# Kernel optimization log

Measured on AMD Instinct MI355X. Metric: run time of the kernel, lower is better.

The kernel has to match this reference:

```python
import jax, jax.numpy as jnp
from jax import lax
import numpy as np

HIDDEN = 64
B, T = 256, 3000


def setup_inputs() -> dict:
    key = jax.random.key(0)
    ks = jax.random.split(key, 7)
    s = 1.0 / np.sqrt(HIDDEN)  # torch default uniform(-1/sqrt(H), 1/sqrt(H))
    u = lambda k, shape: jax.random.uniform(k, shape, jnp.float32, -s, s)
    return {
        "x": jax.random.normal(ks[0], (B, T, 1), dtype=jnp.float32),
        "W_ih": u(ks[1], (3 * HIDDEN, 1)),
        "W_hh": u(ks[2], (3 * HIDDEN, HIDDEN)),
        "b_ih": u(ks[3], (3 * HIDDEN,)),
        "b_hh": u(ks[4], (3 * HIDDEN,)),
        "W_fc": u(ks[5], (1, HIDDEN)),
        "b_fc": u(ks[6], (1,)),
    }


def reference(x, W_ih, W_hh, b_ih, b_hh, W_fc, b_fc):
    # Precompute input contributions to all three gates for all timesteps: (B, T, 3H)
    gi = jnp.einsum("bti,gi->btg", x, W_ih) + b_ih

    def step(h, gi_t):
        gh = h @ W_hh.T + b_hh                      # (B, 3H)
        i_r, i_z, i_n = jnp.split(gi_t, 3, axis=-1)  # torch gate order: r, z, n
        h_r, h_z, h_n = jnp.split(gh, 3, axis=-1)
        r = jax.nn.sigmoid(i_r + h_r)
        z = jax.nn.sigmoid(i_z + h_z)
        n = jnp.tanh(i_n + r * h_n)
        h_new = (1.0 - z) * n + z * h
        return h_new, None

    h0 = jnp.zeros((x.shape[0], HIDDEN), dtype=x.dtype)
    hT, _ = lax.scan(step, h0, jnp.swapaxes(gi, 0, 1))  # scan over T
    # fc(o[:, -1]).squeeze() -> (B,)
    return (hT @ W_fc.T + b_fc).squeeze(-1)
```

## Files before the change

### kernel.cpp

```cpp
#include <hip/hip_runtime.h>
#include <math.h>

#define T_LEN 3000
#define HID 64

typedef _Float16 f16;
typedef f16 f16x8 __attribute__((ext_vector_type(8)));
typedef float f32x4 __attribute__((ext_vector_type(4)));

#define NLOG2E  (-1.4426950408889634f)
#define N2LOG2E (-2.8853900817779268f)

__device__ __forceinline__ float bcast_lane(float v, int j) {
    return __builtin_bit_cast(float,
        __builtin_amdgcn_readlane(__builtin_bit_cast(int, v), j));
}

__global__ __launch_bounds__(256, 1)
void gru_tail(
    const float* __restrict__ x,
    const float* __restrict__ W_ih,
    const float* __restrict__ W_hh,
    const float* __restrict__ b_ih,
    const float* __restrict__ b_hh,
    const float* __restrict__ W_fc,
    const float* __restrict__ b_fc,
    float* __restrict__ out)
{
    const int tid = threadIdx.x;
    const int w   = tid >> 6;
    const int l   = tid & 63;
    const int col = l & 15;
    const int grp = l >> 4;
    const int u   = 16 * w + col;
    const int b   = blockIdx.x;
    const long xbase = (long)b * T_LEN;

    __shared__ __align__(16) f16 hbuf[2][HID];
    __shared__ float hf32[HID];

    f16x8 Bf[3][2];
#pragma unroll
    for (int g = 0; g < 3; ++g) {
#pragma unroll
        for (int hf = 0; hf < 2; ++hf) {
            const float* p = W_hh + (size_t)(64 * g + 16 * w + col) * HID
                           + 8 * grp + 32 * hf;
            const float4 a = *reinterpret_cast<const float4*>(p);
            const float4 c = *reinterpret_cast<const float4*>(p + 4);
            f16x8 v;
            v[0] = (f16)a.x; v[1] = (f16)a.y; v[2] = (f16)a.z; v[3] = (f16)a.w;
            v[4] = (f16)c.x; v[5] = (f16)c.y; v[6] = (f16)c.z; v[7] = (f16)c.w;
            Bf[g][hf] = v;
        }
    }

    const float wihr2 = W_ih[u]        * NLOG2E;
    const float wihz2 = W_ih[64 + u]   * NLOG2E;
    const float wihn2 = W_ih[128 + u]  * N2LOG2E;
    const float br2   = (b_ih[u]        + b_hh[u])        * NLOG2E;
    const float bz2   = (b_ih[64 + u]   + b_hh[64 + u])   * NLOG2E;
    const float bin2  = b_ih[128 + u]  * N2LOG2E;
    const float bhn2  = b_hh[128 + u]  * N2LOG2E;

    float xwin = x[xbase + l];
    float xnxt = (64 + l < T_LEN) ? x[xbase + 64 + l] : 0.0f;

    if (tid < HID) hbuf[0][tid] = (f16)0.0f;
    __syncthreads();

    float h = 0.0f;
    const f32x4 zf = {0.f, 0.f, 0.f, 0.f};

    const f16x8* s0A = reinterpret_cast<const f16x8*>(hbuf[0]) + grp;
    const f16x8* s0B = s0A + 4;
    const f16x8* s1A = reinterpret_cast<const f16x8*>(hbuf[1]) + grp;
    const f16x8* s1B = s1A + 4;
    f16* d0 = &hbuf[0][u];
    f16* d1 = &hbuf[1][u];

    auto step = [&](const f16x8* aP, const f16x8* bP, f16* dstu, int t) {
        const int j = t & 63;

        const f16x8 A0 = *aP;
        const f16x8 A1 = *bP;

        const float xt    = bcast_lane(xwin, j);
        const float pre_r = fmaf(xt, wihr2, br2);
        const float pre_z = fmaf(xt, wihz2, bz2);
        const float pre_n = fmaf(xt, wihn2, bin2);

        f32x4 pr = __builtin_amdgcn_mfma_f32_16x16x32_f16(A0, Bf[0][0], zf, 0, 0, 0);
        f32x4 pz = __builtin_amdgcn_mfma_f32_16x16x32_f16(A0, Bf[1][0], zf, 0, 0, 0);
        f32x4 pn = __builtin_amdgcn_mfma_f32_16x16x32_f16(A0, Bf[2][0], zf, 0, 0, 0);
        f32x4 qr = __builtin_amdgcn_mfma_f32_16x16x32_f16(A1, Bf[0][1], pr, 0, 0, 0);
        f32x4 qz = __builtin_amdgcn_mfma_f32_16x16x32_f16(A1, Bf[1][1], pz, 0, 0, 0);
        f32x4 qn = __builtin_amdgcn_mfma_f32_16x16x32_f16(A1, Bf[2][1], pn, 0, 0, 0);

        const float r = __builtin_amdgcn_rcpf(
            1.0f + __builtin_amdgcn_exp2f(fmaf(qr[0], NLOG2E, pre_r)));
        const float hn2 = fmaf(qn[0], N2LOG2E, bhn2);
        const float z = __builtin_amdgcn_rcpf(
            1.0f + __builtin_amdgcn_exp2f(fmaf(qz[0], NLOG2E, pre_z)));
        const float zh  = z * h;
        const float omz = 1.0f - z;
        const float n = fmaf(2.0f, __builtin_amdgcn_rcpf(
            1.0f + __builtin_amdgcn_exp2f(fmaf(r, hn2, pre_n))), -1.0f);
        h = fmaf(omz, n, zh);

        *dstu = (f16)h;
        if (j == 63) {
            xwin = xnxt;
            const int idx = t + 65 + l;
            xnxt = (idx < T_LEN) ? x[xbase + idx] : 0.0f;
        }
        asm volatile("s_waitcnt lgkmcnt(0)\n\ts_barrier" ::: "memory");
    };

    for (int t = 0; t < T_LEN; t += 2) {
        step(s0A, s0B, d1, t);
        step(s1A, s1B, d0, t + 1);
    }

    hf32[u] = h;
    __syncthreads();
    if (tid < HID) {
        float v = hf32[tid] * W_fc[tid];
#pragma unroll
        for (int off = 32; off > 0; off >>= 1) v += __shfl_down(v, off);
        if (tid == 0) out[b] = v + b_fc[0];
    }
}

extern "C" void kernel_launch(void* const* d_in, const int* in_sizes, int n_in,
                              void* d_out, int out_size, void* d_ws, size_t ws_size,
                              hipStream_t stream) {
    const float* x    = (const float*)d_in[0];
    const float* W_ih = (const float*)d_in[1];
    const float* W_hh = (const float*)d_in[2];
    const float* b_ih = (const float*)d_in[3];
    const float* b_hh = (const float*)d_in[4];
    const float* W_fc = (const float*)d_in[5];
    const float* b_fc = (const float*)d_in[6];
    float* out = (float*)d_out;

    const int B = 256;
    gru_tail<<<B, 256, 0, stream>>>(x, W_ih, W_hh, b_ih, b_hh, W_fc, b_fc, out);
}
```

Before: 636.8 us.

## Replace per-step MFMA matvec with packed fdot2 dot products and quad DPP reduction

```diff
diff --git a/kernel.cpp b/kernel.cpp
--- a/kernel.cpp
+++ b/kernel.cpp
@@ -5,8 +5,8 @@
 #define HID 64
 
 typedef _Float16 f16;
+typedef f16 f16x2 __attribute__((ext_vector_type(2)));
 typedef f16 f16x8 __attribute__((ext_vector_type(8)));
-typedef float f32x4 __attribute__((ext_vector_type(4)));
 
 #define NLOG2E  (-1.4426950408889634f)
 #define N2LOG2E (-2.8853900817779268f)
@@ -16,8 +16,15 @@
         __builtin_amdgcn_readlane(__builtin_bit_cast(int, v), j));
 }
 
+template <int CTRL>
+__device__ __forceinline__ float quad_xor_add(float v) {
+    const int t = __builtin_amdgcn_mov_dpp(
+        __builtin_bit_cast(int, v), CTRL, 0xf, 0xf, true);
+    return v + __builtin_bit_cast(float, t);
+}
+
 __global__ __launch_bounds__(256, 1)
-void gru_tail(
+void gru_qdot(
     const float* __restrict__ x,
     const float* __restrict__ W_ih,
     const float* __restrict__ W_hh,
@@ -30,29 +37,30 @@
     const int tid = threadIdx.x;
     const int w   = tid >> 6;
     const int l   = tid & 63;
-    const int col = l & 15;
-    const int grp = l >> 4;
-    const int u   = 16 * w + col;
+    const int u   = 16 * w + (l >> 2);
+    const int k0  = 16 * (l & 3);
     const int b   = blockIdx.x;
     const long xbase = (long)b * T_LEN;
 
     __shared__ __align__(16) f16 hbuf[2][HID];
     __shared__ float hf32[HID];
 
-    f16x8 Bf[3][2];
+    f16x2 Wd[3][8];
 #pragma unroll
     for (int g = 0; g < 3; ++g) {
-#pragma unroll
-        for (int hf = 0; hf < 2; ++hf) {
-            const float* p = W_hh + (size_t)(64 * g + 16 * w + col) * HID
-                           + 8 * grp + 32 * hf;
-            const float4 a = *reinterpret_cast<const float4*>(p);
-            const float4 c = *reinterpret_cast<const float4*>(p + 4);
-            f16x8 v;
-            v[0] = (f16)a.x; v[1] = (f16)a.y; v[2] = (f16)a.z; v[3] = (f16)a.w;
-            v[4] = (f16)c.x; v[5] = (f16)c.y; v[6] = (f16)c.z; v[7] = (f16)c.w;
-            Bf[g][hf] = v;
-        }
+        const float* p = W_hh + (size_t)(64 * g + u) * HID + k0;
+        const float4 a = *reinterpret_cast<const float4*>(p);
+        const float4 c = *reinterpret_cast<const float4*>(p + 4);
+        const float4 d = *reinterpret_cast<const float4*>(p + 8);
+        const float4 e = *reinterpret_cast<const float4*>(p + 12);
+        Wd[g][0].x = (f16)a.x; Wd[g][0].y = (f16)a.y;
+        Wd[g][1].x = (f16)a.z; Wd[g][1].y = (f16)a.w;
+        Wd[g][2].x = (f16)c.x; Wd[g][2].y = (f16)c.y;
+        Wd[g][3].x = (f16)c.z; Wd[g][3].y = (f16)c.w;
+        Wd[g][4].x = (f16)d.x; Wd[g][4].y = (f16)d.y;
+        Wd[g][5].x = (f16)d.z; Wd[g][5].y = (f16)d.w;
+        Wd[g][6].x = (f16)e.x; Wd[g][6].y = (f16)e.y;
+        Wd[g][7].x = (f16)e.z; Wd[g][7].y = (f16)e.w;
     }
 
     const float wihr2 = W_ih[u]        * NLOG2E;
@@ -70,38 +78,51 @@
     __syncthreads();
 
     float h = 0.0f;
-    const f32x4 zf = {0.f, 0.f, 0.f, 0.f};
 
-    const f16x8* s0A = reinterpret_cast<const f16x8*>(hbuf[0]) + grp;
-    const f16x8* s0B = s0A + 4;
-    const f16x8* s1A = reinterpret_cast<const f16x8*>(hbuf[1]) + grp;
-    const f16x8* s1B = s1A + 4;
+    union HU { f16x8 v8; f16x2 v2[4]; };
+    const f16x8* s0 = reinterpret_cast<const f16x8*>(hbuf[0]) + 2 * (l & 3);
+    const f16x8* s1 = reinterpret_cast<const f16x8*>(hbuf[1]) + 2 * (l & 3);
     f16* d0 = &hbuf[0][u];
     f16* d1 = &hbuf[1][u];
 
-    auto step = [&](const f16x8* aP, const f16x8* bP, f16* dstu, int t) {
+    auto step = [&](const f16x8* srcP, f16* dstu, int t) {
         const int j = t & 63;
 
-        const f16x8 A0 = *aP;
-        const f16x8 A1 = *bP;
+        HU hlo, hhi;
+        hlo.v8 = srcP[0];
+        hhi.v8 = srcP[1];
 
         const float xt    = bcast_lane(xwin, j);
         const float pre_r = fmaf(xt, wihr2, br2);
         const float pre_z = fmaf(xt, wihz2, bz2);
         const float pre_n = fmaf(xt, wihn2, bin2);
 
-        f32x4 pr = __builtin_amdgcn_mfma_f32_16x16x32_f16(A0, Bf[0][0], zf, 0, 0, 0);
-        f32x4 pz = __builtin_amdgcn_mfma_f32_16x16x32_f16(A0, Bf[1][0], zf, 0, 0, 0);
-        f32x4 pn = __builtin_amdgcn_mfma_f32_16x16x32_f16(A0, Bf[2][0], zf, 0, 0, 0);
-        f32x4 qr = __builtin_amdgcn_mfma_f32_16x16x32_f16(A1, Bf[0][1], pr, 0, 0, 0);
-        f32x4 qz = __builtin_amdgcn_mfma_f32_16x16x32_f16(A1, Bf[1][1], pz, 0, 0, 0);
-        f32x4 qn = __builtin_amdgcn_mfma_f32_16x16x32_f16(A1, Bf[2][1], pn, 0, 0, 0);
+        float sr = 0.f, sz = 0.f, sn = 0.f;
+#pragma unroll
+        for (int p = 0; p < 4; ++p) {
+            sr = __builtin_amdgcn_fdot2(Wd[0][p], hlo.v2[p], sr, false);
+            sz = __builtin_amdgcn_fdot2(Wd[1][p], hlo.v2[p], sz, false);
+            sn = __builtin_amdgcn_fdot2(Wd[2][p], hlo.v2[p], sn, false);
+        }
+#pragma unroll
+        for (int p = 0; p < 4; ++p) {
+            sr = __builtin_amdgcn_fdot2(Wd[0][4 + p], hhi.v2[p], sr, false);
+            sz = __builtin_amdgcn_fdot2(Wd[1][4 + p], hhi.v2[p], sz, false);
+            sn = __builtin_amdgcn_fdot2(Wd[2][4 + p], hhi.v2[p], sn, false);
+        }
+
+        sr = quad_xor_add<0xB1>(sr);
+        sz = quad_xor_add<0xB1>(sz);
+        sn = quad_xor_add<0xB1>(sn);
+        sr = quad_xor_add<0x4E>(sr);
+        sz = quad_xor_add<0x4E>(sz);
+        sn = quad_xor_add<0x4E>(sn);
 
         const float r = __builtin_amdgcn_rcpf(
-            1.0f + __builtin_amdgcn_exp2f(fmaf(qr[0], NLOG2E, pre_r)));
-        const float hn2 = fmaf(qn[0], N2LOG2E, bhn2);
+            1.0f + __builtin_amdgcn_exp2f(fmaf(sr, NLOG2E, pre_r)));
+        const float hn2 = fmaf(sn, N2LOG2E, bhn2);
         const float z = __builtin_amdgcn_rcpf(
-            1.0f + __builtin_amdgcn_exp2f(fmaf(qz[0], NLOG2E, pre_z)));
+            1.0f + __builtin_amdgcn_exp2f(fmaf(sz, NLOG2E, pre_z)));
         const float zh  = z * h;
         const float omz = 1.0f - z;
         const float n = fmaf(2.0f, __builtin_amdgcn_rcpf(
@@ -118,8 +139,8 @@
     };
 
     for (int t = 0; t < T_LEN; t += 2) {
-        step(s0A, s0B, d1, t);
-        step(s1A, s1B, d0, t + 1);
+        step(s0, d1, t);
+        step(s1, d0, t + 1);
     }
 
     hf32[u] = h;
@@ -145,5 +166,5 @@
     float* out = (float*)d_out;
 
     const int B = 256;
-    gru_tail<<<B, 256, 0, stream>>>(x, W_ih, W_hh, b_ih, b_hh, W_fc, b_fc, out);
+    gru_qdot<<<B, 256, 0, stream>>>(x, W_ih, W_hh, b_ih, b_hh, W_fc, b_fc, out);
 }
```

Result: slower. 686.4 us (+7.8%).
